# Kernel tuning notes

Measured on AMD Instinct MI355X. Metric: run time of the kernel, lower is better.

Reference implementation:

```python
import jax, jax.numpy as jnp
from jax import lax
import numpy as np

DECAY = 0.5
THRESH = 1.0


def _conv(x, w, b, stride, pad):
    y = lax.conv_general_dilated(
        x, w, window_strides=stride, padding=[(pad, pad), (pad, pad)],
        dimension_numbers=("NCHW", "OIHW", "NCHW"))
    return y + b[None, :, None, None]


def setup_inputs() -> dict:
    key = jax.random.key(0)
    ks = jax.random.split(key, 9)
    T, B = 16, 16
    x_seq = jax.random.uniform(ks[0], (T, B, 1, 100, 768), dtype=jnp.float32)
    # LIF spiking encoder weights
    w1 = jax.random.normal(ks[1], (16, 1, 5, 5), jnp.float32) * 0.2
    b1 = jnp.zeros((16,), jnp.float32)
    w2 = jax.random.normal(ks[2], (32, 16, 3, 3), jnp.float32) * 0.1
    b2 = jnp.zeros((32,), jnp.float32)
    # dense CNN decoder weights
    w3 = jax.random.normal(ks[3], (64, 32, 3, 3), jnp.float32) * 0.06
    b3 = jnp.zeros((64,), jnp.float32)
    w4 = jax.random.normal(ks[4], (1, 64, 3, 3), jnp.float32) * 0.04
    b4 = jnp.zeros((1,), jnp.float32)
    return {"x_seq": x_seq, "w1": w1, "b1": b1, "w2": w2, "b2": b2,
            "w3": w3, "b3": b3, "w4": w4, "b4": b4}


def reference(x_seq, w1, b1, w2, b2, w3, b3, w4, b4):
    B = x_seq.shape[1]
    dt = x_seq.dtype

    def step(carry, x):
        mem1, mem2 = carry
        # LIF layer 1: [B,1,100,768] -> [B,16,50,384]
        mem1 = mem1 * DECAY + _conv(x, w1, b1, (2, 2), 2)
        s1 = (mem1 >= THRESH).astype(dt)
        mem1 = mem1 * (1.0 - s1)  # hard reset
        # LIF layer 2: [B,16,50,384] -> [B,32,25,192]
        mem2 = mem2 * DECAY + _conv(s1, w2, b2, (2, 2), 1)
        s2 = (mem2 >= THRESH).astype(dt)
        mem2 = mem2 * (1.0 - s2)
        return (mem1, mem2), None

    mem1_0 = jnp.zeros((B, 16, 50, 384), dt)
    mem2_0 = jnp.zeros((B, 32, 25, 192), dt)
    (mem1, mem2), _ = lax.scan(step, (mem1_0, mem2_0), x_seq)

    # dense decoder on final membrane potential
    h = jax.nn.relu(_conv(mem2, w3, b3, (1, 1), 1))
    h = _conv(h, w4, b4, (1, 1), 1)  # [B,1,25,192]
    h = jax.image.resize(h, (B, 1, 100, 768), method="bilinear")  # align_corners=False semantics
    return jax.nn.softplus(h)
```

## Files before the change

kernel.cpp:

```cpp
#include <hip/hip_runtime.h>

#define T_STEPS 16
#define BATCH 16
#define XHW (100*768)
#define M2_ELEMS (BATCH*32*25*192)
#define C4_ELEMS (BATCH*25*192)
#define H3_ELEMS (BATCH*64*25*192)

__global__ __launch_bounds__(256) void k_scan(
    const float* __restrict__ x_seq,
    const float* __restrict__ w1,
    const float* __restrict__ b1,
    const float* __restrict__ w2,
    const float* __restrict__ b2,
    float* __restrict__ mem2)
{
    __shared__ float s1s[5][16][72];
    __shared__ float xs[13][136];
    __shared__ float w2s[4608];
    __shared__ float b2s[32];

    const int tid  = threadIdx.x;
    const int bxx  = blockIdx.x;
    const int b    = blockIdx.y;
    const int wseg = bxx / 13;
    const int rg   = bxx % 13;
    const int c0   = wseg * 32;

    for (int i = tid; i < 4608; i += 256) {
        int o = i & 31, r = i >> 5;
        w2s[i] = w2[o * 144 + r];
    }
    if (tid < 32) b2s[tid] = b2[tid];
    for (int i = tid; i < 5 * 16 * 72; i += 256) ((float*)s1s)[i] = 0.f;

    const int ch = tid & 15;
    const int ig = tid >> 4;
    float w1reg[25];
#pragma unroll
    for (int k = 0; k < 25; k++) w1reg[k] = w1[ch * 25 + k];
    const float b1reg = b1[ch];

    const int oc   = tid >> 3;
    const int r2   = (tid >> 2) & 1;
    const int ch4  = tid & 3;
    const int r_out = 2 * rg + r2;
    const bool c2ok = (r_out < 25);
    const float bias2 = b2s[0] * 0.f;

    float m1reg[3][8];
#pragma unroll
    for (int k = 0; k < 3; k++)
#pragma unroll
        for (int c = 0; c < 8; c++) m1reg[k][c] = 0.f;
    float mem2reg[8];
#pragma unroll
    for (int c = 0; c < 8; c++) mem2reg[c] = 0.f;

    for (int t = 0; t < T_STEPS; t++) {
        const float* xb = x_seq + ((size_t)t * BATCH + b) * XHW;
        for (int i = tid; i < 13 * 136; i += 256) {
            int q = i / 136, xc = i % 136;
            int gxr = 8 * rg - 4 + q;
            int gxc = 4 * c0 - 4 + xc;
            float v = 0.f;
            if ((unsigned)gxr < 100u && (unsigned)gxc < 768u) v = xb[gxr * 768 + gxc];
            xs[q][xc] = v;
        }
        __syncthreads();

#pragma unroll
        for (int k = 0; k < 3; k++) {
            int item = ig + 16 * k;
            if (item < 45) {
                int i  = item / 9;
                int cn = item % 9;
                int m  = 4 * rg - 1 + i;
                if (m >= 0 && m <= 49) {
                    float acc[8];
#pragma unroll
                    for (int c = 0; c < 8; c++) acc[c] = b1reg;
#pragma unroll
                    for (int kh = 0; kh < 5; kh++) {
                        const float* xr = &xs[2 * i + kh][16 * cn];
                        float4 v0 = *(const float4*)(xr);
                        float4 v1 = *(const float4*)(xr + 4);
                        float4 v2 = *(const float4*)(xr + 8);
                        float4 v3 = *(const float4*)(xr + 12);
                        float4 v4 = *(const float4*)(xr + 16);
                        float xv[20] = {v0.x, v0.y, v0.z, v0.w,
                                        v1.x, v1.y, v1.z, v1.w,
                                        v2.x, v2.y, v2.z, v2.w,
                                        v3.x, v3.y, v3.z, v3.w,
                                        v4.x, v4.y, v4.z, v4.w};
#pragma unroll
                        for (int kw = 0; kw < 5; kw++) {
                            float w = w1reg[kh * 5 + kw];
#pragma unroll
                            for (int c = 0; c < 8; c++)
                                acc[c] = fmaf(xv[2 * c + kw], w, acc[c]);
                        }
                    }
                    int lcb = 8 * cn;
#pragma unroll
                    for (int c = 0; c < 8; c++) {
                        int lc = lcb + c;
                        int gc = 2 * c0 - 1 + lc;
                        if (lc < 66 && (unsigned)gc < 384u) {
                            float mn = m1reg[k][c] * 0.5f + acc[c];
                            bool f = (mn >= 1.0f);
                            s1s[i][ch][lc] = f ? 1.f : 0.f;
                            m1reg[k][c] = f ? 0.f : mn;
                        }
                    }
                }
            }
        }
        __syncthreads();

        if (c2ok) {
            float acc[8];
#pragma unroll
            for (int c = 0; c < 8; c++) acc[c] = 0.f;
            for (int ic = 0; ic < 16; ic++) {
#pragma unroll
                for (int kh = 0; kh < 3; kh++) {
                    const float* sp = &s1s[2 * r2 + kh][ic][16 * ch4];
                    float4 a0 = *(const float4*)(sp);
                    float4 a1 = *(const float4*)(sp + 4);
                    float4 a2 = *(const float4*)(sp + 8);
                    float4 a3 = *(const float4*)(sp + 12);
                    float4 a4 = *(const float4*)(sp + 16);
                    float sv[20] = {a0.x, a0.y, a0.z, a0.w,
                                    a1.x, a1.y, a1.z, a1.w,
                                    a2.x, a2.y, a2.z, a2.w,
                                    a3.x, a3.y, a3.z, a3.w,
                                    a4.x, a4.y, a4.z, a4.w};
                    const float* wp = &w2s[((ic * 3 + kh) * 3) * 32 + oc];
                    float wk0 = wp[0], wk1 = wp[32], wk2 = wp[64];
#pragma unroll
                    for (int c = 0; c < 8; c++) {
                        float s = fmaf(sv[2 * c], wk0,
                                  fmaf(sv[2 * c + 1], wk1,
                                       sv[2 * c + 2] * wk2));
                        acc[c] += s;
                    }
                }
            }
            float bb = b2s[oc];
#pragma unroll
            for (int c = 0; c < 8; c++) {
                float mn = mem2reg[c] * 0.5f + (acc[c] + bb);
                mem2reg[c] = (mn >= 1.0f) ? 0.f : mn;
            }
        }
        __syncthreads();
    }

    if (c2ok) {
        int base = ((b * 32 + oc) * 25 + r_out) * 192 + c0 + 8 * ch4;
#pragma unroll
        for (int c = 0; c < 8; c++) mem2[base + c] = mem2reg[c];
    }
    (void)bias2;
}

__global__ __launch_bounds__(192) void k3_conv3_relu(
    const float* __restrict__ mem2,
    const float* __restrict__ w3,
    const float* __restrict__ b3,
    float* __restrict__ h)
{
    __shared__ float wsm[288 * 16];
    __shared__ float bsm[16];
    int ocbase = blockIdx.y * 16;
    for (int i = threadIdx.x; i < 4608; i += 192) {
        int o = i & 15, rr = i >> 4;
        wsm[i] = w3[(ocbase + o) * 288 + rr];
    }
    if (threadIdx.x < 16) bsm[threadIdx.x] = b3[ocbase + threadIdx.x];
    __syncthreads();

    int j   = threadIdx.x;
    int bx  = blockIdx.x;
    int b   = bx / 13, ohp = bx % 13;
    int oh0 = ohp * 2;
    bool r1ok = (oh0 + 1) < 25;

    float acc0[16], acc1[16];
#pragma unroll
    for (int o = 0; o < 16; o++) { acc0[o] = bsm[o]; acc1[o] = bsm[o]; }

    const float* mb = mem2 + b * (32 * 25 * 192);
    for (int ic = 0; ic < 32; ic++) {
        const float* mc = mb + ic * (25 * 192);
        float rw[4][3];
#pragma unroll
        for (int q = 0; q < 4; q++) {
            int ih = oh0 - 1 + q;
            bool okh = (unsigned)ih < 25u;
#pragma unroll
            for (int c = 0; c < 3; c++) {
                int iw = j - 1 + c;
                rw[q][c] = (okh && (unsigned)iw < 192u) ? mc[ih * 192 + iw] : 0.f;
            }
        }
#pragma unroll
        for (int kh = 0; kh < 3; kh++) {
#pragma unroll
            for (int kw = 0; kw < 3; kw++) {
                const float4* wp = (const float4*)&wsm[((ic * 3 + kh) * 3 + kw) * 16];
                float v0 = rw[kh][kw], v1 = rw[kh + 1][kw];
#pragma unroll
                for (int g = 0; g < 4; g++) {
                    float4 wv = wp[g];
                    acc0[g*4+0] = fmaf(v0, wv.x, acc0[g*4+0]);
                    acc0[g*4+1] = fmaf(v0, wv.y, acc0[g*4+1]);
                    acc0[g*4+2] = fmaf(v0, wv.z, acc0[g*4+2]);
                    acc0[g*4+3] = fmaf(v0, wv.w, acc0[g*4+3]);
                    acc1[g*4+0] = fmaf(v1, wv.x, acc1[g*4+0]);
                    acc1[g*4+1] = fmaf(v1, wv.y, acc1[g*4+1]);
                    acc1[g*4+2] = fmaf(v1, wv.z, acc1[g*4+2]);
                    acc1[g*4+3] = fmaf(v1, wv.w, acc1[g*4+3]);
                }
            }
        }
    }
#pragma unroll
    for (int o = 0; o < 16; o++) {
        int idx = ((b * 64 + ocbase + o) * 25 + oh0) * 192 + j;
        h[idx] = fmaxf(acc0[o], 0.f);
        if (r1ok) h[idx + 192] = fmaxf(acc1[o], 0.f);
    }
}

__global__ __launch_bounds__(256) void k4_conv4(
    const float* __restrict__ h,
    const float* __restrict__ w4,
    float* __restrict__ c4)
{
    __shared__ float wsm[144];
    int icbase = blockIdx.y * 16;
    for (int i = threadIdx.x; i < 144; i += 256) wsm[i] = w4[icbase * 9 + i];
    __syncthreads();

    int gid = blockIdx.x * 256 + threadIdx.x;
    int ow = gid % 192;
    int t2 = gid / 192;
    int oh = t2 % 25;
    int b  = t2 / 25;

    float acc = 0.f;
    const float* hb = h + (b * 64 + icbase) * (25 * 192);
    for (int ic = 0; ic < 16; ic++) {
        const float* hc = hb + ic * (25 * 192);
#pragma unroll
        for (int kh = 0; kh < 3; kh++) {
            int ih = oh - 1 + kh;
            bool okh = (unsigned)ih < 25u;
#pragma unroll
            for (int kw = 0; kw < 3; kw++) {
                int iw = ow - 1 + kw;
                float v = (okh && (unsigned)iw < 192u) ? hc[ih * 192 + iw] : 0.f;
                acc = fmaf(v, wsm[ic * 9 + kh * 3 + kw], acc);
            }
        }
    }
    atomicAdd(&c4[gid], acc);
}

__global__ __launch_bounds__(256) void k5_resize_softplus(
    const float* __restrict__ c4,
    const float* __restrict__ b4,
    float* __restrict__ out)
{
    int gid = blockIdx.x * 256 + threadIdx.x;
    int ox = gid % 768;
    int t2 = gid / 768;
    int oy = t2 % 100;
    int b  = t2 / 100;

    float bias = b4[0];
    float sy = (oy + 0.5f) * 0.25f - 0.5f;
    float sx = (ox + 0.5f) * 0.25f - 0.5f;
    int y0 = (int)floorf(sy); float fy = sy - (float)y0;
    int x0 = (int)floorf(sx); float fx = sx - (float)x0;
    int y1 = y0 + 1, x1 = x0 + 1;
    y0 = y0 < 0 ? 0 : (y0 > 24 ? 24 : y0);
    y1 = y1 < 0 ? 0 : (y1 > 24 ? 24 : y1);
    x0 = x0 < 0 ? 0 : (x0 > 191 ? 191 : x0);
    x1 = x1 < 0 ? 0 : (x1 > 191 ? 191 : x1);

    const float* cb = c4 + b * 4800;
    float v00 = cb[y0 * 192 + x0] + bias, v01 = cb[y0 * 192 + x1] + bias;
    float v10 = cb[y1 * 192 + x0] + bias, v11 = cb[y1 * 192 + x1] + bias;
    float v = (1.f - fy) * ((1.f - fx) * v00 + fx * v01)
            +        fy  * ((1.f - fx) * v10 + fx * v11);
    out[gid] = fmaxf(v, 0.f) + log1pf(expf(-fabsf(v)));
}

extern "C" void kernel_launch(void* const* d_in, const int* in_sizes, int n_in,
                              void* d_out, int out_size, void* d_ws, size_t ws_size,
                              hipStream_t stream) {
    const float* x_seq = (const float*)d_in[0];
    const float* w1 = (const float*)d_in[1];
    const float* b1 = (const float*)d_in[2];
    const float* w2 = (const float*)d_in[3];
    const float* b2 = (const float*)d_in[4];
    const float* w3 = (const float*)d_in[5];
    const float* b3 = (const float*)d_in[6];
    const float* w4 = (const float*)d_in[7];
    const float* b4 = (const float*)d_in[8];
    float* out = (float*)d_out;

    float* ws   = (float*)d_ws;
    float* mem2 = ws;
    float* c4o  = ws + M2_ELEMS;
    float* h    = ws + M2_ELEMS + C4_ELEMS;

    hipMemsetAsync(c4o, 0, (size_t)C4_ELEMS * sizeof(float), stream);

    k_scan<<<dim3(78, 16), 256, 0, stream>>>(x_seq, w1, b1, w2, b2, mem2);
    k3_conv3_relu<<<dim3(16 * 13, 4), 192, 0, stream>>>(mem2, w3, b3, h);
    k4_conv4<<<dim3(300, 4), 256, 0, stream>>>(h, w4, c4o);
    k5_resize_softplus<<<4800, 256, 0, stream>>>(c4o, b4, out);
}
```

Baseline: 789.1 us.

## Read conv1 input directly from global and remap conv2 threads to share spike rows

New measurement: 1.194 ms. 1.51x slower.

```diff
diff --git a/kernel.cpp b/kernel.cpp
--- a/kernel.cpp
+++ b/kernel.cpp
@@ -15,10 +15,8 @@
     const float* __restrict__ b2,
     float* __restrict__ mem2)
 {
-    __shared__ float s1s[5][16][72];
-    __shared__ float xs[13][136];
-    __shared__ float w2s[4608];
-    __shared__ float b2s[32];
+    __shared__ float s1s[5][16][76];
+    __shared__ float w2s[32 * 196];
 
     const int tid  = threadIdx.x;
     const int bxx  = blockIdx.x;
@@ -27,12 +25,12 @@
     const int rg   = bxx % 13;
     const int c0   = wseg * 32;
 
-    for (int i = tid; i < 4608; i += 256) {
-        int o = i & 31, r = i >> 5;
-        w2s[i] = w2[o * 144 + r];
-    }
-    if (tid < 32) b2s[tid] = b2[tid];
-    for (int i = tid; i < 5 * 16 * 72; i += 256) ((float*)s1s)[i] = 0.f;
+    for (int idx = tid; idx < 6144; idx += 256) {
+        int o = idx / 192, r = idx % 192;
+        int icc = r / 12, kk = r % 12;
+        w2s[o * 196 + icc * 12 + kk] = (kk < 9) ? w2[o * 144 + icc * 9 + kk] : 0.f;
+    }
+    for (int i = tid; i < 5 * 16 * 76; i += 256) ((float*)s1s)[i] = 0.f;
 
     const int ch = tid & 15;
     const int ig = tid >> 4;
@@ -41,128 +39,146 @@
     for (int k = 0; k < 25; k++) w1reg[k] = w1[ch * 25 + k];
     const float b1reg = b1[ch];
 
-    const int oc   = tid >> 3;
-    const int r2   = (tid >> 2) & 1;
-    const int ch4  = tid & 3;
-    const int r_out = 2 * rg + r2;
-    const bool c2ok = (r_out < 25);
-    const float bias2 = b2s[0] * 0.f;
+    int it_i[3], it_cn[3];
+    bool it_ok[3];
+#pragma unroll
+    for (int k = 0; k < 3; k++) {
+        int item = ig + 16 * k;
+        int i = item / 9, cn = item % 9;
+        int m = 4 * rg - 1 + i;
+        it_i[k] = i; it_cn[k] = cn;
+        it_ok[k] = (item < 45) && (m >= 0) && (m <= 49);
+    }
+
+    const int oc = tid >> 3;
+    const int cg = tid & 7;
+    const float bb = b2[oc];
+    const float* wrow = &w2s[oc * 196];
 
     float m1reg[3][8];
 #pragma unroll
     for (int k = 0; k < 3; k++)
 #pragma unroll
         for (int c = 0; c < 8; c++) m1reg[k][c] = 0.f;
-    float mem2reg[8];
-#pragma unroll
-    for (int c = 0; c < 8; c++) mem2reg[c] = 0.f;
+    float m2r[2][4];
+#pragma unroll
+    for (int r = 0; r < 2; r++)
+#pragma unroll
+        for (int c = 0; c < 4; c++) m2r[r][c] = 0.f;
+
+    __syncthreads();
+
+    const float4 z4 = make_float4(0.f, 0.f, 0.f, 0.f);
 
     for (int t = 0; t < T_STEPS; t++) {
         const float* xb = x_seq + ((size_t)t * BATCH + b) * XHW;
-        for (int i = tid; i < 13 * 136; i += 256) {
-            int q = i / 136, xc = i % 136;
-            int gxr = 8 * rg - 4 + q;
-            int gxc = 4 * c0 - 4 + xc;
-            float v = 0.f;
-            if ((unsigned)gxr < 100u && (unsigned)gxc < 768u) v = xb[gxr * 768 + gxc];
-            xs[q][xc] = v;
+
+#pragma unroll
+        for (int k = 0; k < 3; k++) {
+            if (!it_ok[k]) continue;
+            int i = it_i[k], cn = it_cn[k];
+            int lcb = 8 * cn;
+            int xcb = 4 * c0 + 16 * cn - 4;
+            float acc[8];
+#pragma unroll
+            for (int c = 0; c < 8; c++) acc[c] = b1reg;
+#pragma unroll
+            for (int kh = 0; kh < 5; kh++) {
+                int xr = 8 * rg - 4 + 2 * i + kh;
+                bool rok = (unsigned)xr < 100u;
+                const float* xp = &xb[xr * 768];
+                float4 v[5];
+#pragma unroll
+                for (int j = 0; j < 5; j++) {
+                    int colj = xcb + 4 * j;
+                    bool ok = rok && (colj >= 0) && (colj <= 764);
+                    v[j] = ok ? *(const float4*)&xp[colj] : z4;
+                }
+                float xv[20] = {v[0].x, v[0].y, v[0].z, v[0].w,
+                                v[1].x, v[1].y, v[1].z, v[1].w,
+                                v[2].x, v[2].y, v[2].z, v[2].w,
+                                v[3].x, v[3].y, v[3].z, v[3].w,
+                                v[4].x, v[4].y, v[4].z, v[4].w};
+#pragma unroll
+                for (int kw = 0; kw < 5; kw++) {
+                    float w = w1reg[kh * 5 + kw];
+#pragma unroll
+                    for (int c = 0; c < 8; c++)
+                        acc[c] = fmaf(xv[2 * c + kw], w, acc[c]);
+                }
+            }
+            float out[8];
+#pragma unroll
+            for (int c = 0; c < 8; c++) {
+                int lc = lcb + c;
+                int gc = 2 * c0 - 1 + lc;
+                bool valid = (lc < 66) && (gc >= 0) && (gc < 384);
+                float mn = m1reg[k][c] * 0.5f + acc[c];
+                bool f = (mn >= 1.0f);
+                out[c] = (f && valid) ? 1.f : 0.f;
+                if (valid) m1reg[k][c] = f ? 0.f : mn;
+            }
+            float* dst = &s1s[i][ch][lcb];
+            *(float4*)dst       = make_float4(out[0], out[1], out[2], out[3]);
+            *(float4*)(dst + 4) = make_float4(out[4], out[5], out[6], out[7]);
         }
         __syncthreads();
 
-#pragma unroll
-        for (int k = 0; k < 3; k++) {
-            int item = ig + 16 * k;
-            if (item < 45) {
-                int i  = item / 9;
-                int cn = item % 9;
-                int m  = 4 * rg - 1 + i;
-                if (m >= 0 && m <= 49) {
-                    float acc[8];
-#pragma unroll
-                    for (int c = 0; c < 8; c++) acc[c] = b1reg;
-#pragma unroll
-                    for (int kh = 0; kh < 5; kh++) {
-                        const float* xr = &xs[2 * i + kh][16 * cn];
-                        float4 v0 = *(const float4*)(xr);
-                        float4 v1 = *(const float4*)(xr + 4);
-                        float4 v2 = *(const float4*)(xr + 8);
-                        float4 v3 = *(const float4*)(xr + 12);
-                        float4 v4 = *(const float4*)(xr + 16);
-                        float xv[20] = {v0.x, v0.y, v0.z, v0.w,
-                                        v1.x, v1.y, v1.z, v1.w,
-                                        v2.x, v2.y, v2.z, v2.w,
-                                        v3.x, v3.y, v3.z, v3.w,
-                                        v4.x, v4.y, v4.z, v4.w};
-#pragma unroll
-                        for (int kw = 0; kw < 5; kw++) {
-                            float w = w1reg[kh * 5 + kw];
-#pragma unroll
-                            for (int c = 0; c < 8; c++)
-                                acc[c] = fmaf(xv[2 * c + kw], w, acc[c]);
-                        }
+        {
+            float acc0[4] = {0.f, 0.f, 0.f, 0.f};
+            float acc1[4] = {0.f, 0.f, 0.f, 0.f};
+#pragma unroll
+            for (int ic = 0; ic < 16; ic++) {
+                const float* wr = &wrow[ic * 12];
+                float4 wa = *(const float4*)wr;
+                float4 wb2 = *(const float4*)(wr + 4);
+                float wq[9] = {wa.x, wa.y, wa.z, wa.w,
+                               wb2.x, wb2.y, wb2.z, wb2.w, wr[8]};
+#pragma unroll
+                for (int i = 0; i < 5; i++) {
+                    const float* sp = &s1s[i][ic][8 * cg];
+                    float4 a = *(const float4*)sp;
+                    float4 d = *(const float4*)(sp + 4);
+                    float4 e = *(const float4*)(sp + 8);
+                    float sv[12] = {a.x, a.y, a.z, a.w,
+                                    d.x, d.y, d.z, d.w,
+                                    e.x, e.y, e.z, e.w};
+                    if (i < 3) {
+                        float k0 = wq[i * 3], k1 = wq[i * 3 + 1], k2 = wq[i * 3 + 2];
+#pragma unroll
+                        for (int c = 0; c < 4; c++)
+                            acc0[c] += fmaf(sv[2 * c], k0,
+                                       fmaf(sv[2 * c + 1], k1, sv[2 * c + 2] * k2));
                     }
-                    int lcb = 8 * cn;
-#pragma unroll
-                    for (int c = 0; c < 8; c++) {
-                        int lc = lcb + c;
-                        int gc = 2 * c0 - 1 + lc;
-                        if (lc < 66 && (unsigned)gc < 384u) {
-                            float mn = m1reg[k][c] * 0.5f + acc[c];
-                            bool f = (mn >= 1.0f);
-                            s1s[i][ch][lc] = f ? 1.f : 0.f;
-                            m1reg[k][c] = f ? 0.f : mn;
-                        }
+                    if (i >= 2) {
+                        int kk = (i - 2) * 3;
+                        float k0 = wq[kk], k1 = wq[kk + 1], k2 = wq[kk + 2];
+#pragma unroll
+                        for (int c = 0; c < 4; c++)
+                            acc1[c] += fmaf(sv[2 * c], k0,
+                                       fmaf(sv[2 * c + 1], k1, sv[2 * c + 2] * k2));
                     }
                 }
             }
+#pragma unroll
+            for (int c = 0; c < 4; c++) {
+                float mn0 = m2r[0][c] * 0.5f + (acc0[c] + bb);
+                m2r[0][c] = (mn0 >= 1.0f) ? 0.f : mn0;
+                float mn1 = m2r[1][c] * 0.5f + (acc1[c] + bb);
+                m2r[1][c] = (mn1 >= 1.0f) ? 0.f : mn1;
+            }
         }
         __syncthreads();
-
-        if (c2ok) {
-            float acc[8];
-#pragma unroll
-            for (int c = 0; c < 8; c++) acc[c] = 0.f;
-            for (int ic = 0; ic < 16; ic++) {
-#pragma unroll
-                for (int kh = 0; kh < 3; kh++) {
-                    const float* sp = &s1s[2 * r2 + kh][ic][16 * ch4];
-                    float4 a0 = *(const float4*)(sp);
-                    float4 a1 = *(const float4*)(sp + 4);
-                    float4 a2 = *(const float4*)(sp + 8);
-                    float4 a3 = *(const float4*)(sp + 12);
-                    float4 a4 = *(const float4*)(sp + 16);
-                    float sv[20] = {a0.x, a0.y, a0.z, a0.w,
-                                    a1.x, a1.y, a1.z, a1.w,
-                                    a2.x, a2.y, a2.z, a2.w,
-                                    a3.x, a3.y, a3.z, a3.w,
-                                    a4.x, a4.y, a4.z, a4.w};
-                    const float* wp = &w2s[((ic * 3 + kh) * 3) * 32 + oc];
-                    float wk0 = wp[0], wk1 = wp[32], wk2 = wp[64];
-#pragma unroll
-                    for (int c = 0; c < 8; c++) {
-                        float s = fmaf(sv[2 * c], wk0,
-                                  fmaf(sv[2 * c + 1], wk1,
-                                       sv[2 * c + 2] * wk2));
-                        acc[c] += s;
-                    }
-                }
-            }
-            float bb = b2s[oc];
-#pragma unroll
-            for (int c = 0; c < 8; c++) {
-                float mn = mem2reg[c] * 0.5f + (acc[c] + bb);
-                mem2reg[c] = (mn >= 1.0f) ? 0.f : mn;
-            }
-        }
-        __syncthreads();
-    }
-
-    if (c2ok) {
-        int base = ((b * 32 + oc) * 25 + r_out) * 192 + c0 + 8 * ch4;
-#pragma unroll
-        for (int c = 0; c < 8; c++) mem2[base + c] = mem2reg[c];
-    }
-    (void)bias2;
+    }
+
+    {
+        int cb = c0 + 4 * cg;
+        int base = ((b * 32 + oc) * 25 + 2 * rg) * 192 + cb;
+        *(float4*)&mem2[base] = make_float4(m2r[0][0], m2r[0][1], m2r[0][2], m2r[0][3]);
+        if (2 * rg + 1 < 25)
+            *(float4*)&mem2[base + 192] =
+                make_float4(m2r[1][0], m2r[1][1], m2r[1][2], m2r[1][3]);
+    }
 }
 
 __global__ __launch_bounds__(192) void k3_conv3_relu(
```
